# Optimization experiments

Measured on AMD Instinct MI355X. Metric: run time of the kernel, lower is better.

## Reference

```python
import jax, jax.numpy as jnp
import numpy as np

DIM = 64
V_CH = 5
N_CONTRASTS = 4
IMG = 224
P = IMG * IMG  # num_v_patches
B = 32
TEMPERATURE = 10.0
EPS_LN = 1e-5
EPS_NORM = 1e-8


def _mlp_ln(x, W1, b1, W2, b2, g, beta):
    # x: (..., DIM) -> Linear(DIM,128) -> LeakyReLU(0.1) -> Linear(128,16) -> LayerNorm(16)
    h = jax.nn.leaky_relu(x @ W1 + b1, negative_slope=0.1)
    h = h @ W2 + b2
    mu = h.mean(-1, keepdims=True)
    var = ((h - mu) ** 2).mean(-1, keepdims=True)
    return (h - mu) * jax.lax.rsqrt(var + EPS_LN) * g + beta


def setup_inputs() -> dict:
    key = jax.random.key(0)
    ks = jax.random.split(key, 16)
    q = jax.random.normal(ks[0], (B, DIM, 1), jnp.float32)
    k = jax.random.normal(ks[1], (B, DIM, 1, N_CONTRASTS), jnp.float32)
    v = jax.random.normal(ks[2], (B, V_CH, P, N_CONTRASTS), jnp.float32)
    mask = (jax.random.uniform(ks[3], (B, 1, IMG, IMG, N_CONTRASTS)) > 0.5).astype(jnp.float32)
    modality_dropout = jax.random.randint(ks[4], (B, N_CONTRASTS), 0, 2, jnp.int32)

    def lin(kk, fan_in, fan_out):
        lim = 1.0 / np.sqrt(fan_in)
        k1, k2 = jax.random.split(kk)
        W = jax.random.uniform(k1, (fan_in, fan_out), jnp.float32, -lim, lim)
        b = jax.random.uniform(k2, (fan_out,), jnp.float32, -lim, lim)
        return W, b

    Wq1, bq1 = lin(ks[5], DIM, 128)
    Wq2, bq2 = lin(ks[6], 128, 16)
    Wk1, bk1 = lin(ks[7], DIM, 128)
    Wk2, bk2 = lin(ks[8], 128, 16)
    gq = jnp.ones((16,), jnp.float32); betaq = jnp.zeros((16,), jnp.float32)
    gk = jnp.ones((16,), jnp.float32); betak = jnp.zeros((16,), jnp.float32)
    return {
        'q': q, 'k': k, 'v': v, 'mask': mask, 'modality_dropout': modality_dropout,
        'Wq1': Wq1, 'bq1': bq1, 'Wq2': Wq2, 'bq2': bq2, 'gq': gq, 'betaq': betaq,
        'Wk1': Wk1, 'bk1': bk1, 'Wk2': Wk2, 'bk2': bk2, 'gk': gk, 'betak': betak,
    }


def reference(q, k, v, mask, modality_dropout,
              Wq1, bq1, Wq2, bq2, gq, betaq,
              Wk1, bk1, Wk2, bk2, gk, betak):
    scale = DIM ** (-0.5)
    # q: (B, DIM, 1) -> (B, DIM)
    q16 = _mlp_ln(q[:, :, 0], Wq1, bq1, Wq2, bq2, gq, betaq)          # (B, 16)
    # k: (B, DIM, 1, C) -> (B, C, DIM)
    kf = jnp.transpose(k, (0, 2, 3, 1))[:, 0]                          # (B, C, DIM)
    k16 = _mlp_ln(kf, Wk1, bk1, Wk2, bk2, gk, betak)                   # (B, C, 16)
    # scalar logit per (batch, contrast); num_q_patches == 1
    logits = jnp.einsum('bd,bcd->bc', q16, k16) * scale                # (B, C)
    md = modality_dropout.astype(logits.dtype)
    logits = logits - md * 1.0e5
    att = jax.nn.softmax(logits / TEMPERATURE, axis=-1)                # (B, C)
    # broadcast to image grid (torch code repeats the 1x1 map to IMG x IMG)
    att_map = att[:, None, None, :] * mask[:, 0]                       # (B, IMG, IMG, C)
    # normalize_and_smooth_attention: renormalize over contrasts after masking
    att_norm = att_map / (att_map.sum(-1, keepdims=True) + EPS_NORM)   # (B, IMG, IMG, C)
    # weighted sum of value logits over contrasts
    v_pcv = jnp.transpose(v, (0, 2, 3, 1))                             # (B, P, C, V_CH)
    fused = jnp.einsum('bpc,bpcv->bpv', att_norm.reshape(-1, P, N_CONTRASTS), v_pcv)
    fused = jnp.transpose(fused.reshape(-1, IMG, IMG, V_CH), (0, 3, 1, 2))  # (B, V_CH, IMG, IMG)
    attention = jnp.transpose(att_norm, (0, 3, 1, 2))                  # (B, C, IMG, IMG)
    return fused, attention
```

## Files before the change

kernel.cpp:

```cpp
#include <hip/hip_runtime.h>

#define DIM 64
#define H1  128
#define H2  16
#define NC  4
#define VCH 5
#define IMG 224
#define PP  (IMG * IMG)
#define BB  32

__global__ __launch_bounds__(128) void mlp_kernel(
    const float* __restrict__ q, const float* __restrict__ k,
    const float* __restrict__ Wq1, const float* __restrict__ bq1,
    const float* __restrict__ Wq2, const float* __restrict__ bq2,
    const float* __restrict__ gq,  const float* __restrict__ betaq,
    const float* __restrict__ Wk1, const float* __restrict__ bk1,
    const float* __restrict__ Wk2, const float* __restrict__ bk2,
    const float* __restrict__ gk,  const float* __restrict__ betak,
    float* __restrict__ ws)
{
    __shared__ float xs[DIM];
    __shared__ float sh1[H1];
    __shared__ float sh2[H2];

    const int row = blockIdx.x;
    const int tid = threadIdx.x;
    const bool isq = (row < BB);

    const float *W1, *b1, *W2, *b2, *g, *beta;
    int b, c;
    if (isq) {
        b = row; c = 0;
        W1 = Wq1; b1 = bq1; W2 = Wq2; b2 = bq2; g = gq; beta = betaq;
    } else {
        const int idx = row - BB;
        b = idx >> 2; c = idx & 3;
        W1 = Wk1; b1 = bk1; W2 = Wk2; b2 = bk2; g = gk; beta = betak;
    }

    if (tid < DIM) {
        xs[tid] = isq ? q[b * DIM + tid] : k[(b * DIM + tid) * NC + c];
    }
    __syncthreads();

    float acc = b1[tid];
#pragma unroll 8
    for (int d = 0; d < DIM; ++d)
        acc = fmaf(xs[d], W1[d * H1 + tid], acc);
    sh1[tid] = (acc > 0.0f) ? acc : 0.1f * acc;
    __syncthreads();

    if (tid < H2) {
        float a2 = b2[tid];
#pragma unroll 8
        for (int i = 0; i < H1; ++i)
            a2 = fmaf(sh1[i], W2[i * H2 + tid], a2);
        sh2[tid] = a2;
    }
    __syncthreads();

    if (tid < H2) {
        float mu = 0.0f;
#pragma unroll
        for (int j = 0; j < H2; ++j) mu += sh2[j];
        mu *= (1.0f / H2);
        float var = 0.0f;
#pragma unroll
        for (int j = 0; j < H2; ++j) { float d0 = sh2[j] - mu; var += d0 * d0; }
        var *= (1.0f / H2);
        const float y = (sh2[tid] - mu) * rsqrtf(var + 1e-5f) * g[tid] + beta[tid];
        float* out = isq ? (ws + b * H2) : (ws + BB * H2 + (b * NC + c) * H2);
        out[tid] = y;
    }
}

__global__ __launch_bounds__(256) void fuse_kernel(
    const float* __restrict__ v, const float* __restrict__ mask,
    const int* __restrict__ md, const float* __restrict__ ws,
    float* __restrict__ out_fused, float* __restrict__ out_attn)
{
    __shared__ float l_s[NC];
    __shared__ float att_s[NC];

    const int bid = blockIdx.x;
    const int b   = bid / (PP / 256);
    const int p   = (bid % (PP / 256)) * 256 + threadIdx.x;

    if (threadIdx.x < NC) {
        const int c = threadIdx.x;
        const float* q16 = ws + b * H2;
        const float* k16 = ws + BB * H2 + (b * NC + c) * H2;
        float dot = 0.0f;
#pragma unroll
        for (int j = 0; j < H2; ++j) dot = fmaf(q16[j], k16[j], dot);
        const float logit = dot * 0.125f - (float)md[b * NC + c] * 1.0e5f;
        l_s[c] = logit * 0.1f;
    }
    __syncthreads();
    if (threadIdx.x < NC) {
        const int c = threadIdx.x;
        const float m = fmaxf(fmaxf(l_s[0], l_s[1]), fmaxf(l_s[2], l_s[3]));
        const float e = __expf(l_s[c] - m);
        const float s = __expf(l_s[0] - m) + __expf(l_s[1] - m) +
                        __expf(l_s[2] - m) + __expf(l_s[3] - m);
        att_s[c] = e / s;
    }
    __syncthreads();

    const float4 mk = *reinterpret_cast<const float4*>(mask + (size_t)(b * PP + p) * NC);
    float a0 = att_s[0] * mk.x;
    float a1 = att_s[1] * mk.y;
    float a2 = att_s[2] * mk.z;
    float a3 = att_s[3] * mk.w;
    const float inv = 1.0f / (a0 + a1 + a2 + a3 + 1e-8f);
    a0 *= inv; a1 *= inv; a2 *= inv; a3 *= inv;

    const size_t ab = (size_t)b * NC * PP + p;
    __builtin_nontemporal_store(a0, out_attn + ab);
    __builtin_nontemporal_store(a1, out_attn + ab + PP);
    __builtin_nontemporal_store(a2, out_attn + ab + 2 * PP);
    __builtin_nontemporal_store(a3, out_attn + ab + 3 * PP);

    const size_t vb = (size_t)b * VCH * PP + p;
#pragma unroll
    for (int vc = 0; vc < VCH; ++vc) {
        const float* vp = v + (vb + (size_t)vc * PP) * NC;
        float vx = __builtin_nontemporal_load(vp);
        float vy = __builtin_nontemporal_load(vp + 1);
        float vz = __builtin_nontemporal_load(vp + 2);
        float vw = __builtin_nontemporal_load(vp + 3);
        const float f = a0 * vx + a1 * vy + a2 * vz + a3 * vw;
        __builtin_nontemporal_store(f, out_fused + vb + (size_t)vc * PP);
    }
}

extern "C" void kernel_launch(void* const* d_in, const int* in_sizes, int n_in,
                              void* d_out, int out_size, void* d_ws, size_t ws_size,
                              hipStream_t stream) {
    const float* q     = (const float*)d_in[0];
    const float* k     = (const float*)d_in[1];
    const float* v     = (const float*)d_in[2];
    const float* mask  = (const float*)d_in[3];
    const int*   md    = (const int*)  d_in[4];
    const float* Wq1   = (const float*)d_in[5];
    const float* bq1   = (const float*)d_in[6];
    const float* Wq2   = (const float*)d_in[7];
    const float* bq2   = (const float*)d_in[8];
    const float* gq    = (const float*)d_in[9];
    const float* betaq = (const float*)d_in[10];
    const float* Wk1   = (const float*)d_in[11];
    const float* bk1   = (const float*)d_in[12];
    const float* Wk2   = (const float*)d_in[13];
    const float* bk2   = (const float*)d_in[14];
    const float* gk    = (const float*)d_in[15];
    const float* betak = (const float*)d_in[16];

    float* ws        = (float*)d_ws;
    float* out_fused = (float*)d_out;
    float* out_attn  = out_fused + (size_t)BB * VCH * PP;

    hipLaunchKernelGGL(mlp_kernel, dim3(BB + BB * NC), dim3(128), 0, stream,
                       q, k, Wq1, bq1, Wq2, bq2, gq, betaq,
                       Wk1, bk1, Wk2, bk2, gk, betak, ws);

    hipLaunchKernelGGL(fuse_kernel, dim3(BB * (PP / 256)), dim3(256), 0, stream,
                       v, mask, md, ws, out_fused, out_attn);
}
```

Measured before the change: 252.9 us.

## Precompute softmax in separate kernel; vectorize nontemporal loads in fuse kernel

Moves the per-batch logit dot product and softmax into a small single-block kernel that writes attention weights to the workspace, which removes two __syncthreads and the serial setup work from every fuse block. The fuse kernel now reads the four weights directly and loads both the mask and v as 16-byte nontemporal vector loads instead of scalar nontemporal loads. The cost is an extra kernel launch and a dependency through global memory.

```diff
diff --git a/kernel.cpp b/kernel.cpp
--- a/kernel.cpp
+++ b/kernel.cpp
@@ -8,6 +8,9 @@
 #define IMG 224
 #define PP  (IMG * IMG)
 #define BB  32
+
+typedef float f4 __attribute__((ext_vector_type(4)));
+
 
 __global__ __launch_bounds__(128) void mlp_kernel(
     const float* __restrict__ q, const float* __restrict__ k,
@@ -74,44 +77,45 @@
     }
 }
 
+__global__ __launch_bounds__(128) void att_kernel(
+    const int* __restrict__ md, float* __restrict__ ws)
+{
+    const int tid = threadIdx.x;
+    const int b = tid >> 2, c = tid & 3;
+    const float* q16 = ws + b * H2;
+    const float* k16 = ws + BB * H2 + tid * H2;
+    float dot = 0.0f;
+#pragma unroll
+    for (int j = 0; j < H2; ++j) dot = fmaf(q16[j], k16[j], dot);
+    float l = (dot * 0.125f - (float)md[tid] * 1.0e5f) * 0.1f;
+    float m = l;
+    m = fmaxf(m, __shfl_xor(m, 1, 64));
+    m = fmaxf(m, __shfl_xor(m, 2, 64));
+    float e = __expf(l - m);
+    float s = e;
+    s += __shfl_xor(s, 1, 64);
+    s += __shfl_xor(s, 2, 64);
+    ws[BB * H2 + BB * NC * H2 + tid] = e / s;
+}
+
 __global__ __launch_bounds__(256) void fuse_kernel(
     const float* __restrict__ v, const float* __restrict__ mask,
-    const int* __restrict__ md, const float* __restrict__ ws,
+    const float* __restrict__ ws,
     float* __restrict__ out_fused, float* __restrict__ out_attn)
 {
-    __shared__ float l_s[NC];
-    __shared__ float att_s[NC];
-
     const int bid = blockIdx.x;
     const int b   = bid / (PP / 256);
     const int p   = (bid % (PP / 256)) * 256 + threadIdx.x;
 
-    if (threadIdx.x < NC) {
-        const int c = threadIdx.x;
-        const float* q16 = ws + b * H2;
-        const float* k16 = ws + BB * H2 + (b * NC + c) * H2;
-        float dot = 0.0f;
-#pragma unroll
-        for (int j = 0; j < H2; ++j) dot = fmaf(q16[j], k16[j], dot);
-        const float logit = dot * 0.125f - (float)md[b * NC + c] * 1.0e5f;
-        l_s[c] = logit * 0.1f;
-    }
-    __syncthreads();
-    if (threadIdx.x < NC) {
-        const int c = threadIdx.x;
-        const float m = fmaxf(fmaxf(l_s[0], l_s[1]), fmaxf(l_s[2], l_s[3]));
-        const float e = __expf(l_s[c] - m);
-        const float s = __expf(l_s[0] - m) + __expf(l_s[1] - m) +
-                        __expf(l_s[2] - m) + __expf(l_s[3] - m);
-        att_s[c] = e / s;
-    }
-    __syncthreads();
+    const float* att = ws + BB * H2 + BB * NC * H2 + b * NC;
+    const float t0 = att[0], t1 = att[1], t2 = att[2], t3 = att[3];
 
-    const float4 mk = *reinterpret_cast<const float4*>(mask + (size_t)(b * PP + p) * NC);
-    float a0 = att_s[0] * mk.x;
-    float a1 = att_s[1] * mk.y;
-    float a2 = att_s[2] * mk.z;
-    float a3 = att_s[3] * mk.w;
+    const f4 mk = __builtin_nontemporal_load(
+        reinterpret_cast<const f4*>(mask + (size_t)(b * PP + p) * NC));
+    float a0 = t0 * mk.x;
+    float a1 = t1 * mk.y;
+    float a2 = t2 * mk.z;
+    float a3 = t3 * mk.w;
     const float inv = 1.0f / (a0 + a1 + a2 + a3 + 1e-8f);
     a0 *= inv; a1 *= inv; a2 *= inv; a3 *= inv;
 
@@ -124,12 +128,9 @@
     const size_t vb = (size_t)b * VCH * PP + p;
 #pragma unroll
     for (int vc = 0; vc < VCH; ++vc) {
-        const float* vp = v + (vb + (size_t)vc * PP) * NC;
-        float vx = __builtin_nontemporal_load(vp);
-        float vy = __builtin_nontemporal_load(vp + 1);
-        float vz = __builtin_nontemporal_load(vp + 2);
-        float vw = __builtin_nontemporal_load(vp + 3);
-        const float f = a0 * vx + a1 * vy + a2 * vz + a3 * vw;
+        const f4 vv = __builtin_nontemporal_load(
+            reinterpret_cast<const f4*>(v + (vb + (size_t)vc * PP) * NC));
+        const float f = a0 * vv.x + a1 * vv.y + a2 * vv.z + a3 * vv.w;
         __builtin_nontemporal_store(f, out_fused + vb + (size_t)vc * PP);
     }
 }
@@ -163,6 +164,8 @@
                        q, k, Wq1, bq1, Wq2, bq2, gq, betaq,
                        Wk1, bk1, Wk2, bk2, gk, betak, ws);
 
+    hipLaunchKernelGGL(att_kernel, dim3(1), dim3(128), 0, stream, md, ws);
+
     hipLaunchKernelGGL(fuse_kernel, dim3(BB * (PP / 256)), dim3(256), 0, stream,
-                       v, mask, md, ws, out_fused, out_attn);
+                       v, mask, ws, out_fused, out_attn);
 }
```

After: 247.4 us. 2.1% less time.
